# Kernel optimization log

Hardware: AMD Instinct MI355X
Metric: run time of the kernel (lower is better)

Reference implementation:

```python
import jax, jax.numpy as jnp
import numpy as np

N = 100000      # nodes
E = 1600000     # directed edges
F_IN = 128      # input features
H = 64          # hidden_channels
C = 32          # num_classes


def setup_inputs() -> dict:
    key = jax.random.key(0)
    ks = jax.random.split(key, 8)
    x = jax.random.normal(ks[0], (N, F_IN), jnp.float32)
    edge_index = jax.random.randint(ks[1], (2, E), 0, N, jnp.int32)
    W1 = jax.random.normal(ks[2], (F_IN, H), jnp.float32) * (1.0 / np.sqrt(F_IN))
    b1 = jnp.zeros((H,), jnp.float32)
    W2 = jax.random.normal(ks[3], (H, H), jnp.float32) * (1.0 / np.sqrt(H))
    b2 = jnp.zeros((H,), jnp.float32)
    Wout = jax.random.normal(ks[4], (H, C), jnp.float32) * (1.0 / np.sqrt(H))
    bout = jnp.zeros((C,), jnp.float32)
    return {"x": x, "edge_index": edge_index, "W1": W1, "b1": b1,
            "W2": W2, "b2": b2, "Wout": Wout, "bout": bout}


def gcn_conv(x, W, b, src, dst, n):
    """PyG GCNConv: out = D^-1/2 (A + I) D^-1/2 (X W) + b,
    with degree computed on A + I."""
    h = x @ W  # [N, out]
    ones = jnp.ones(dst.shape[0], h.dtype)
    deg = jax.ops.segment_sum(ones, dst, num_segments=n) + 1.0  # self-loop
    dinv = jax.lax.rsqrt(deg)                                   # [N]
    coef = dinv[src] * dinv[dst]                                # [E]
    agg = jax.ops.segment_sum(h[src] * coef[:, None], dst, num_segments=n)
    agg = agg + h * (dinv * dinv)[:, None]                      # self-loop message
    return agg + b


def reference(x, edge_index, W1, b1, W2, b2, Wout, bout):
    src, dst = edge_index[0], edge_index[1]
    n = x.shape[0]
    h = jax.nn.relu(gcn_conv(x, W1, b1, src, dst, n))
    # dropout(p=0.5) is a no-op in eval mode
    h = jax.nn.relu(gcn_conv(h, W2, b2, src, dst, n))
    return jax.nn.softmax(h @ Wout + bout, axis=1)
```

## Files before the change

kernel.cpp:

```cpp
#include <hip/hip_runtime.h>
#include <stdint.h>


typedef unsigned short u16;
typedef unsigned int u32;
typedef __attribute__((ext_vector_type(8))) short bf16x8;
typedef __attribute__((ext_vector_type(4))) float f32x4;

#define GN 100000
#define GE 1600000
#define NBKT 196
#define CBLK 782

__device__ __forceinline__ float bf2f(u32 lo16) {
  union { u32 i; float f; } v; v.i = lo16 << 16; return v.f;
}
__device__ __forceinline__ u16 f2bf(float f) {
  union { float f; u32 i; } v; v.f = f;
  u32 x = v.i;
  u32 r = x + 0x7fffu + ((x >> 16) & 1u);
  return (u16)(r >> 16);
}
__device__ __forceinline__ u32 pack2(float a, float b) {
  return (u32)f2bf(a) | ((u32)f2bf(b) << 16);
}

__global__ __launch_bounds__(256) void k_detect(const u16* __restrict__ xs,
                                                int* __restrict__ flag,
                                                int* __restrict__ ccount) {
  __shared__ int cnt;
  if (threadIdx.x == 0) cnt = 0;
  if (threadIdx.x < NBKT) ccount[threadIdx.x] = 0;
  __syncthreads();
  int w = 0;
#pragma unroll
  for (int i = 0; i < 16; i++) {
    int s = threadIdx.x * 16 + i;
    u32 u = xs[(size_t)s * 1562];
    u32 ex = (u >> 7) & 0xffu;
    if (ex == 0xffu || ex < 0x40u) w++;
  }
  atomicAdd(&cnt, w);
  __syncthreads();
  if (threadIdx.x == 0) flag[0] = (cnt >= 64) ? 0 : 1;
}

__global__ __launch_bounds__(256) void k_coarse(const int* __restrict__ dst,
                                                int* __restrict__ ccount, int E,
                                                const void* p2, const void* p3,
                                                const void* p4, const void* p5,
                                                const void* p6, const void* p7,
                                                const int* __restrict__ flag,
                                                float* __restrict__ Wf,
                                                u16* __restrict__ Wb1,
                                                u16* __restrict__ Wb2,
                                                u16* __restrict__ Wbo) {
  int tid = threadIdx.x;
  if (blockIdx.x >= CBLK) {
    int i = (blockIdx.x - CBLK) * 256 + tid;
    bool isbf = flag[0] != 0;
    if (i < 14496) {
      const void* src; int off;
      if (i < 8192)       { src = p2; off = i; }
      else if (i < 8256)  { src = p3; off = i - 8192; }
      else if (i < 12352) { src = p4; off = i - 8256; }
      else if (i < 12416) { src = p5; off = i - 12352; }
      else if (i < 14464) { src = p6; off = i - 12416; }
      else                { src = p7; off = i - 14464; }
      Wf[i] = isbf ? bf2f((u32)((const u16*)src)[off]) : ((const float*)src)[off];
    } else if (i < 14496 + 12288) {
      int idx = i - 14496;
      const void* W; u16* dstp;
      if (idx < 8192) { W = p2; dstp = Wb1; }
      else            { W = p4; dstp = Wb2; idx -= 8192; }
      int j  = idx & 7;
      int l  = (idx >> 3) & 63;
      int c  = (idx >> 9) & 3;
      int kc = idx >> 11;
      int k = kc * 32 + (l >> 4) * 8 + j;
      int n = c * 16 + (l & 15);
      dstp[idx] = isbf ? ((const u16*)W)[k * 64 + n]
                       : f2bf(((const float*)W)[k * 64 + n]);
    } else if (i < 14496 + 12288 + 2048) {
      int idx = i - 14496 - 12288;
      int j  = idx & 7;
      int l  = (idx >> 3) & 63;
      int c  = (idx >> 9) & 1;
      int kc = idx >> 10;
      int k = kc * 32 + (l >> 4) * 8 + j;
      int n = c * 16 + (l & 15);
      Wbo[idx] = isbf ? ((const u16*)p6)[k * 32 + n]
                      : f2bf(((const float*)p6)[k * 32 + n]);
    }
    return;
  }
  __shared__ int hist[256];
  hist[tid] = 0;
  __syncthreads();
  int e0 = (blockIdx.x * 256 + tid) * 8;
  if (e0 + 8 <= E) {
    const int4* dp = (const int4*)(dst + e0);
    int4 a = dp[0], b = dp[1];
    atomicAdd(&hist[a.x >> 9], 1); atomicAdd(&hist[a.y >> 9], 1);
    atomicAdd(&hist[a.z >> 9], 1); atomicAdd(&hist[a.w >> 9], 1);
    atomicAdd(&hist[b.x >> 9], 1); atomicAdd(&hist[b.y >> 9], 1);
    atomicAdd(&hist[b.z >> 9], 1); atomicAdd(&hist[b.w >> 9], 1);
  } else {
    for (int q = 0; q < 8 && e0 + q < E; q++)
      atomicAdd(&hist[dst[e0 + q] >> 9], 1);
  }
  __syncthreads();
  if (tid < NBKT && hist[tid]) atomicAdd(&ccount[tid], hist[tid]);
}

__global__ __launch_bounds__(256) void k_cscan(const int* __restrict__ ccount,
                                               int* __restrict__ cbase,
                                               int* __restrict__ cfill) {
  __shared__ int lds[256];
  int tid = threadIdx.x;
  int v = (tid < NBKT) ? ccount[tid] : 0;
  lds[tid] = v;
  __syncthreads();
#pragma unroll
  for (int off = 1; off < 256; off <<= 1) {
    int a = (tid >= off) ? lds[tid - off] : 0;
    __syncthreads();
    lds[tid] += a;
    __syncthreads();
  }
  int excl = lds[tid] - v;
  if (tid < NBKT) { cbase[tid] = excl; cfill[tid] = excl; }
  if (tid == 255) cbase[NBKT] = lds[255];
}

__global__ __launch_bounds__(256) void k_partA(const int* __restrict__ src,
                                               const int* __restrict__ dst,
                                               int* __restrict__ cfill,
                                               u32* __restrict__ pairs, int E) {
  __shared__ int hist[256];
  __shared__ int off[256];
  int tid = threadIdx.x;
  hist[tid] = 0;
  __syncthreads();
  int e0 = (blockIdx.x * 256 + tid) * 8;
  int s_[8], d_[8];
  int cnt = 0;
  if (e0 + 8 <= E) {
    const int4* sp = (const int4*)(src + e0);
    const int4* dp = (const int4*)(dst + e0);
#pragma unroll
    for (int q = 0; q < 2; q++) {
      int4 sv = sp[q], dv = dp[q];
      s_[4 * q + 0] = sv.x; s_[4 * q + 1] = sv.y;
      s_[4 * q + 2] = sv.z; s_[4 * q + 3] = sv.w;
      d_[4 * q + 0] = dv.x; d_[4 * q + 1] = dv.y;
      d_[4 * q + 2] = dv.z; d_[4 * q + 3] = dv.w;
    }
    cnt = 8;
  } else {
    for (int q = 0; q < 8 && e0 + q < E; q++) {
      s_[q] = src[e0 + q]; d_[q] = dst[e0 + q]; cnt++;
    }
  }
  for (int q = 0; q < cnt; q++) atomicAdd(&hist[d_[q] >> 9], 1);
  __syncthreads();
  if (tid < NBKT && hist[tid] > 0) off[tid] = atomicAdd(&cfill[tid], hist[tid]);
  __syncthreads();
  for (int q = 0; q < cnt; q++) {
    int bkt = d_[q] >> 9;
    int pos = atomicAdd(&off[bkt], 1);
    pairs[pos] = ((u32)s_[q] << 9) | ((u32)d_[q] & 511u);
  }
}

__global__ __launch_bounds__(256) void k_partB(const u32* __restrict__ pairs,
                                               const int* __restrict__ cbase,
                                               int* __restrict__ rp,
                                               float* __restrict__ dinv,
                                               int* __restrict__ ssort, int N) {
  __shared__ int cnt[512];
  __shared__ int sc[256];
  int b = blockIdx.x;
  int tid = threadIdx.x;
  int nb0 = b << 9;
  int beg = cbase[b], end = cbase[b + 1];
  cnt[tid] = 0; cnt[tid + 256] = 0;
  __syncthreads();
  for (int i = beg + tid; i < end; i += 256) {
    u32 p = pairs[i];
    atomicAdd(&cnt[p & 511u], 1);
  }
  __syncthreads();
  int c0 = cnt[2 * tid], c1 = cnt[2 * tid + 1];
  int s = c0 + c1;
  sc[tid] = s;
  __syncthreads();
#pragma unroll
  for (int off = 1; off < 256; off <<= 1) {
    int a = (tid >= off) ? sc[tid - off] : 0;
    __syncthreads();
    sc[tid] += a;
    __syncthreads();
  }
  int excl = sc[tid] - s;
  cnt[2 * tid] = excl;
  cnt[2 * tid + 1] = excl + c0;
  int n0 = nb0 + 2 * tid, n1 = n0 + 1;
  if (n0 < N) { rp[n0] = beg + excl;      dinv[n0] = rsqrtf((float)c0 + 1.0f); }
  if (n1 < N) { rp[n1] = beg + excl + c0; dinv[n1] = rsqrtf((float)c1 + 1.0f); }
  if (b == NBKT - 1 && tid == 0) rp[N] = end;
  __syncthreads();
  for (int i = beg + tid; i < end; i += 256) {
    u32 p = pairs[i];
    int pos = beg + atomicAdd(&cnt[p & 511u], 1);
    ssort[pos] = (int)(p >> 9);
  }
}

template <int K, int XMODE>
__global__ __launch_bounds__(256) void k_mgemm(const void* __restrict__ X,
                                               const u16* __restrict__ Wb,
                                               const float* __restrict__ dinv,
                                               const int* __restrict__ flag,
                                               u16* __restrict__ out, int M) {
  constexpr int NKC = K / 32;
  constexpr int P = K + 8;
  __shared__ u16 Bs[NKC * 4 * 64 * 8];
  __shared__ u16 As[128 * P];
  int tid = threadIdx.x;
  bool isbf = (XMODE == 1) ? true : (flag[0] != 0);
#pragma unroll
  for (int i = 0; i < NKC; i++)
    ((uint4*)Bs)[i * 256 + tid] = ((const uint4*)Wb)[i * 256 + tid];

  int rowbase = blockIdx.x * 128;
  int rowsValid = M - rowbase; if (rowsValid > 128) rowsValid = 128;
  if (isbf) {
    constexpr int F8 = K / 8;
    constexpr int NL = K / 16;
    const uint4* Xg = (const uint4*)X;
    uint4 v[NL];
#pragma unroll
    for (int i = 0; i < NL; i++) {
      int q = i * 256 + tid;
      int row = q / F8, c8 = q % F8;
      v[i] = (row < rowsValid) ? Xg[(size_t)(rowbase + row) * F8 + c8]
                               : make_uint4(0, 0, 0, 0);
    }
#pragma unroll
    for (int i = 0; i < NL; i++) {
      int q = i * 256 + tid;
      int row = q / F8, c8 = q % F8;
      *(uint4*)&As[row * P + c8 * 8] = v[i];
    }
  } else {
    constexpr int F4 = K / 4;
    constexpr int NL = K / 8;
    const float4* Xg = (const float4*)X;
    float4 v[NL];
#pragma unroll
    for (int i = 0; i < NL; i++) {
      int q = i * 256 + tid;
      int row = q / F4, c4 = q % F4;
      v[i] = (row < rowsValid) ? Xg[(size_t)(rowbase + row) * F4 + c4]
                               : make_float4(0.f, 0.f, 0.f, 0.f);
    }
#pragma unroll
    for (int i = 0; i < NL; i++) {
      int q = i * 256 + tid;
      int row = q / F4, c4 = q % F4;
      u32* d = (u32*)&As[row * P + c4 * 4];
      d[0] = pack2(v[i].x, v[i].y);
      d[1] = pack2(v[i].z, v[i].w);
    }
  }
  __syncthreads();

  int lane = tid & 63, wave = tid >> 6;
  int m0 = lane & 15;
  int koff = (lane >> 4) * 8;
  f32x4 acc[2][4];
#pragma unroll
  for (int t = 0; t < 2; t++)
#pragma unroll
    for (int c = 0; c < 4; c++) acc[t][c] = (f32x4){0.f, 0.f, 0.f, 0.f};

#pragma unroll
  for (int kc = 0; kc < NKC; kc++) {
    union { uint4 v; bf16x8 s; } a[2];
#pragma unroll
    for (int t = 0; t < 2; t++) {
      int rl = wave * 32 + t * 16 + m0;
      a[t].v = *(const uint4*)&As[rl * P + kc * 32 + koff];
    }
#pragma unroll
    for (int c = 0; c < 4; c++) {
      bf16x8 b = *(const bf16x8*)&Bs[((kc * 4 + c) * 64 + lane) * 8];
      acc[0][c] = __builtin_amdgcn_mfma_f32_16x16x32_bf16(a[0].s, b, acc[0][c], 0, 0, 0);
      acc[1][c] = __builtin_amdgcn_mfma_f32_16x16x32_bf16(a[1].s, b, acc[1][c], 0, 0, 0);
    }
  }
  __syncthreads();
  int cl = lane & 15, rq = (lane >> 4) * 4;
#pragma unroll
  for (int t = 0; t < 2; t++)
#pragma unroll
    for (int reg = 0; reg < 4; reg++) {
      int rl = wave * 32 + t * 16 + rq + reg;
      int r = rowbase + rl;
      float s = (r < M) ? dinv[r] : 0.f;
#pragma unroll
      for (int c = 0; c < 4; c++)
        As[rl * P + c * 16 + cl] = f2bf(acc[t][c][reg] * s);
    }
  __syncthreads();
  uint4* outg = (uint4*)out;
#pragma unroll
  for (int i = 0; i < 4; i++) {
    int q = i * 256 + tid;
    int row = q >> 3, c8 = q & 7;
    int r = rowbase + row;
    if (r < M) outg[(size_t)r * 8 + c8] = *(uint4*)&As[row * P + c8 * 8];
  }
}

__global__ __launch_bounds__(256) void k_pull(const u16* __restrict__ g,
                                              const int* __restrict__ rp,
                                              const int* __restrict__ ss,
                                              const float* __restrict__ dinv,
                                              const float* __restrict__ bias,
                                              u16* __restrict__ out, int N) {
  int gt = blockIdx.x * 256 + threadIdx.x;
  int node = gt >> 3;
  int fq = gt & 7;
  if (node >= N) return;
  const uint4* gp4 = (const uint4*)g;
  int beg = rp[node], end = rp[node + 1];

  uint4 sv = gp4[(size_t)node * 8 + fq];
  float acc[8];
  acc[0] = bf2f(sv.x & 0xffffu); acc[1] = bf2f(sv.x >> 16);
  acc[2] = bf2f(sv.y & 0xffffu); acc[3] = bf2f(sv.y >> 16);
  acc[4] = bf2f(sv.z & 0xffffu); acc[5] = bf2f(sv.z >> 16);
  acc[6] = bf2f(sv.w & 0xffffu); acc[7] = bf2f(sv.w >> 16);

#define ACC8(v)                                                      \
  do {                                                               \
    acc[0] += bf2f((v).x & 0xffffu); acc[1] += bf2f((v).x >> 16);    \
    acc[2] += bf2f((v).y & 0xffffu); acc[3] += bf2f((v).y >> 16);    \
    acc[4] += bf2f((v).z & 0xffffu); acc[5] += bf2f((v).z >> 16);    \
    acc[6] += bf2f((v).w & 0xffffu); acc[7] += bf2f((v).w >> 16);    \
  } while (0)

  int e = beg;
  for (; e + 4 <= end; e += 4) {
    int i0 = ss[e], i1 = ss[e + 1], i2 = ss[e + 2], i3 = ss[e + 3];
    uint4 v0 = gp4[(size_t)i0 * 8 + fq];
    uint4 v1 = gp4[(size_t)i1 * 8 + fq];
    uint4 v2 = gp4[(size_t)i2 * 8 + fq];
    uint4 v3 = gp4[(size_t)i3 * 8 + fq];
    ACC8(v0); ACC8(v1); ACC8(v2); ACC8(v3);
  }
  for (; e < end; e++) {
    int i0 = ss[e];
    uint4 v0 = gp4[(size_t)i0 * 8 + fq];
    ACC8(v0);
  }
#undef ACC8

  float dv = dinv[node];
  float4 b0 = ((const float4*)bias)[fq * 2];
  float4 b1 = ((const float4*)bias)[fq * 2 + 1];
  float r0 = fmaxf(dv * acc[0] + b0.x, 0.f);
  float r1 = fmaxf(dv * acc[1] + b0.y, 0.f);
  float r2 = fmaxf(dv * acc[2] + b0.z, 0.f);
  float r3 = fmaxf(dv * acc[3] + b0.w, 0.f);
  float r4 = fmaxf(dv * acc[4] + b1.x, 0.f);
  float r5 = fmaxf(dv * acc[5] + b1.y, 0.f);
  float r6 = fmaxf(dv * acc[6] + b1.z, 0.f);
  float r7 = fmaxf(dv * acc[7] + b1.w, 0.f);
  ((uint4*)out)[(size_t)node * 8 + fq] =
      make_uint4(pack2(r0, r1), pack2(r2, r3), pack2(r4, r5), pack2(r6, r7));
}

__global__ __launch_bounds__(256) void k_out(const u16* __restrict__ act,
                                             const u16* __restrict__ Wbo,
                                             const float* __restrict__ bof,
                                             const int* __restrict__ flag,
                                             void* __restrict__ outv, int N) {
  constexpr int P = 72;
  __shared__ u16 Bs[2 * 2 * 64 * 8];
  __shared__ u16 As[128 * P];
  __shared__ float Bsh[32];
  int tid = threadIdx.x;
  ((uint4*)Bs)[tid] = ((const uint4*)Wbo)[tid];
  if (tid < 32) Bsh[tid] = bof[tid];

  int rowbase = blockIdx.x * 128;
  int rowsValid = N - rowbase; if (rowsValid > 128) rowsValid = 128;
  const uint4* Xg = (const uint4*)act;
#pragma unroll
  for (int i = 0; i < 4; i++) {
    int q = i * 256 + tid;
    int row = q >> 3, c8 = q & 7;
    uint4 v = (row < rowsValid) ? Xg[(size_t)(rowbase + row) * 8 + c8]
                                : make_uint4(0, 0, 0, 0);
    *(uint4*)&As[row * P + c8 * 8] = v;
  }
  __syncthreads();

  bool isbf = flag[0] != 0;
  int lane = tid & 63, wave = tid >> 6;
  int m0 = lane & 15;
  int koff = (lane >> 4) * 8;
  f32x4 acc[2][2];
#pragma unroll
  for (int t = 0; t < 2; t++)
#pragma unroll
    for (int c = 0; c < 2; c++) acc[t][c] = (f32x4){0.f, 0.f, 0.f, 0.f};

#pragma unroll
  for (int kc = 0; kc < 2; kc++) {
    union { uint4 v; bf16x8 s; } a[2];
#pragma unroll
    for (int t = 0; t < 2; t++) {
      int rl = wave * 32 + t * 16 + m0;
      a[t].v = *(const uint4*)&As[rl * P + kc * 32 + koff];
    }
#pragma unroll
    for (int c = 0; c < 2; c++) {
      bf16x8 b = *(const bf16x8*)&Bs[((kc * 2 + c) * 64 + lane) * 8];
      acc[0][c] = __builtin_amdgcn_mfma_f32_16x16x32_bf16(a[0].s, b, acc[0][c], 0, 0, 0);
      acc[1][c] = __builtin_amdgcn_mfma_f32_16x16x32_bf16(a[1].s, b, acc[1][c], 0, 0, 0);
    }
  }
  int cl = lane & 15, rq = (lane >> 4) * 4;
  float b0 = Bsh[cl], b1 = Bsh[16 + cl];
#pragma unroll
  for (int t = 0; t < 2; t++)
#pragma unroll
    for (int reg = 0; reg < 4; reg++) {
      int r = rowbase + wave * 32 + t * 16 + rq + reg;
      float v0 = acc[t][0][reg] + b0;
      float v1 = acc[t][1][reg] + b1;
      float mx = fmaxf(v0, v1);
      mx = fmaxf(mx, __shfl_xor(mx, 1));
      mx = fmaxf(mx, __shfl_xor(mx, 2));
      mx = fmaxf(mx, __shfl_xor(mx, 4));
      mx = fmaxf(mx, __shfl_xor(mx, 8));
      float e0 = __expf(v0 - mx), e1 = __expf(v1 - mx);
      float s = e0 + e1;
      s += __shfl_xor(s, 1);
      s += __shfl_xor(s, 2);
      s += __shfl_xor(s, 4);
      s += __shfl_xor(s, 8);
      float inv = 1.f / s;
      if (r < N) {
        if (isbf) {
          u16* go = (u16*)outv;
          go[(size_t)r * 32 + cl]      = f2bf(e0 * inv);
          go[(size_t)r * 32 + 16 + cl] = f2bf(e1 * inv);
        } else {
          float* go = (float*)outv;
          go[(size_t)r * 32 + cl]      = e0 * inv;
          go[(size_t)r * 32 + 16 + cl] = e1 * inv;
        }
      }
    }
}

extern "C" void kernel_launch(void* const* d_in, const int* in_sizes, int n_in,
                              void* d_out, int out_size, void* d_ws, size_t ws_size,
                              hipStream_t stream) {
  (void)in_sizes; (void)n_in; (void)out_size; (void)ws_size;
  const void* x  = d_in[0];
  const int* ei  = (const int*)d_in[1];
  const int N = GN, E = GE;
  const int* srcI = ei;
  const int* dstI = ei + E;

  char* ws = (char*)d_ws;
  int*   flag   = (int*)(ws + 0);
  int*   ccount = (int*)(ws + 256);
  int*   cbase  = (int*)(ws + 1088);
  int*   cfill  = (int*)(ws + 1920);
  int*   rp     = (int*)(ws + 4096);
  float* dinv   = (float*)(ws + 404224);
  float* Wf     = (float*)(ws + 804352);
  u16*   Wb1    = (u16*)(ws + 862464);
  u16*   Wb2    = (u16*)(ws + 878848);
  u16*   Wbo    = (u16*)(ws + 887040);
  int*   ssort  = (int*)(ws + 891136);
  u32*   pairs  = (u32*)(ws + 7291136);
  u16*   gA     = (u16*)(ws + 7291136);
  u16*   gB     = (u16*)(ws + 20091136);

  float* b1f = Wf + 8192;
  float* b2f = Wf + 12352;
  float* bof = Wf + 14464;

  k_detect<<<1, 256, 0, stream>>>((const u16*)x, flag, ccount);
  k_coarse<<<CBLK + 113, 256, 0, stream>>>(dstI, ccount, E,
                                           d_in[2], d_in[3], d_in[4], d_in[5],
                                           d_in[6], d_in[7], flag,
                                           Wf, Wb1, Wb2, Wbo);
  k_cscan<<<1, 256, 0, stream>>>(ccount, cbase, cfill);
  k_partA<<<782, 256, 0, stream>>>(srcI, dstI, cfill, pairs, E);
  k_partB<<<NBKT, 256, 0, stream>>>(pairs, cbase, rp, dinv, ssort, N);

  k_mgemm<128, 0><<<782, 256, 0, stream>>>(x, Wb1, dinv, flag, gA, N);
  k_pull<<<3125, 256, 0, stream>>>(gA, rp, ssort, dinv, b1f, gB, N);
  k_mgemm<64, 1><<<782, 256, 0, stream>>>(gB, Wb2, dinv, flag, gA, N);
  k_pull<<<3125, 256, 0, stream>>>(gA, rp, ssort, dinv, b2f, gB, N);
  k_out<<<782, 256, 0, stream>>>(gB, Wbo, bof, flag, d_out, N);
}
```

Baseline: 269.0 us.

## Fixed-capacity buckets and fuse pull aggregation with following GEMM and softmax

Replaces the coarse histogram, scan and partition sequence with a single pass that writes into fixed-capacity buckets (BCAP per bucket), so two kernels and a global sync disappear. It also fuses each neighbor aggregation with the next dense transform: layer 1 pull feeds a 64x64 MFMA that is scaled by dinv and stored, and layer 2 pull feeds the output GEMM plus softmax. This removes the separate mgemm/out launches and the round trips of intermediate activations through memory. The cost is a bucket-overflow risk if a bucket exceeds the fixed capacity, padded row-pointer indexing, and MODE 1 leaving half the waves idle during its MFMA step.

```diff
diff --git a/kernel.cpp b/kernel.cpp
--- a/kernel.cpp
+++ b/kernel.cpp
@@ -10,7 +10,8 @@
 #define GN 100000
 #define GE 1600000
 #define NBKT 196
-#define CBLK 782
+#define BCAP 10240
+#define EBLK 782
 
 __device__ __forceinline__ float bf2f(u32 lo16) {
   union { u32 i; float f; } v; v.i = lo16 << 16; return v.f;
@@ -45,29 +46,31 @@
   if (threadIdx.x == 0) flag[0] = (cnt >= 64) ? 0 : 1;
 }
 
-__global__ __launch_bounds__(256) void k_coarse(const int* __restrict__ dst,
-                                                int* __restrict__ ccount, int E,
-                                                const void* p2, const void* p3,
-                                                const void* p4, const void* p5,
-                                                const void* p6, const void* p7,
-                                                const int* __restrict__ flag,
-                                                float* __restrict__ Wf,
-                                                u16* __restrict__ Wb1,
-                                                u16* __restrict__ Wb2,
-                                                u16* __restrict__ Wbo) {
+__global__ __launch_bounds__(256) void k_partA(const int* __restrict__ src,
+                                               const int* __restrict__ dst,
+                                               int* __restrict__ ccount, int E,
+                                               const void* p2, const void* p3,
+                                               const void* p4, const void* p5,
+                                               const void* p6, const void* p7,
+                                               const int* __restrict__ flag,
+                                               float* __restrict__ Wf,
+                                               u16* __restrict__ Wb1,
+                                               u16* __restrict__ Wb2,
+                                               u16* __restrict__ Wbo,
+                                               u32* __restrict__ pairs) {
   int tid = threadIdx.x;
-  if (blockIdx.x >= CBLK) {
-    int i = (blockIdx.x - CBLK) * 256 + tid;
+  if (blockIdx.x >= EBLK) {
+    int i = (blockIdx.x - EBLK) * 256 + tid;
     bool isbf = flag[0] != 0;
     if (i < 14496) {
-      const void* src; int off;
-      if (i < 8192)       { src = p2; off = i; }
-      else if (i < 8256)  { src = p3; off = i - 8192; }
-      else if (i < 12352) { src = p4; off = i - 8256; }
-      else if (i < 12416) { src = p5; off = i - 12352; }
-      else if (i < 14464) { src = p6; off = i - 12416; }
-      else                { src = p7; off = i - 14464; }
-      Wf[i] = isbf ? bf2f((u32)((const u16*)src)[off]) : ((const float*)src)[off];
+      const void* sp; int off;
+      if (i < 8192)       { sp = p2; off = i; }
+      else if (i < 8256)  { sp = p3; off = i - 8192; }
+      else if (i < 12352) { sp = p4; off = i - 8256; }
+      else if (i < 12416) { sp = p5; off = i - 12352; }
+      else if (i < 14464) { sp = p6; off = i - 12416; }
+      else                { sp = p7; off = i - 14464; }
+      Wf[i] = isbf ? bf2f((u32)((const u16*)sp)[off]) : ((const float*)sp)[off];
     } else if (i < 14496 + 12288) {
       int idx = i - 14496;
       const void* W; u16* dstp;
@@ -95,51 +98,7 @@
     return;
   }
   __shared__ int hist[256];
-  hist[tid] = 0;
-  __syncthreads();
-  int e0 = (blockIdx.x * 256 + tid) * 8;
-  if (e0 + 8 <= E) {
-    const int4* dp = (const int4*)(dst + e0);
-    int4 a = dp[0], b = dp[1];
-    atomicAdd(&hist[a.x >> 9], 1); atomicAdd(&hist[a.y >> 9], 1);
-    atomicAdd(&hist[a.z >> 9], 1); atomicAdd(&hist[a.w >> 9], 1);
-    atomicAdd(&hist[b.x >> 9], 1); atomicAdd(&hist[b.y >> 9], 1);
-    atomicAdd(&hist[b.z >> 9], 1); atomicAdd(&hist[b.w >> 9], 1);
-  } else {
-    for (int q = 0; q < 8 && e0 + q < E; q++)
-      atomicAdd(&hist[dst[e0 + q] >> 9], 1);
-  }
-  __syncthreads();
-  if (tid < NBKT && hist[tid]) atomicAdd(&ccount[tid], hist[tid]);
-}
-
-__global__ __launch_bounds__(256) void k_cscan(const int* __restrict__ ccount,
-                                               int* __restrict__ cbase,
-                                               int* __restrict__ cfill) {
-  __shared__ int lds[256];
-  int tid = threadIdx.x;
-  int v = (tid < NBKT) ? ccount[tid] : 0;
-  lds[tid] = v;
-  __syncthreads();
-#pragma unroll
-  for (int off = 1; off < 256; off <<= 1) {
-    int a = (tid >= off) ? lds[tid - off] : 0;
-    __syncthreads();
-    lds[tid] += a;
-    __syncthreads();
-  }
-  int excl = lds[tid] - v;
-  if (tid < NBKT) { cbase[tid] = excl; cfill[tid] = excl; }
-  if (tid == 255) cbase[NBKT] = lds[255];
-}
-
-__global__ __launch_bounds__(256) void k_partA(const int* __restrict__ src,
-                                               const int* __restrict__ dst,
-                                               int* __restrict__ cfill,
-                                               u32* __restrict__ pairs, int E) {
-  __shared__ int hist[256];
   __shared__ int off[256];
-  int tid = threadIdx.x;
   hist[tid] = 0;
   __syncthreads();
   int e0 = (blockIdx.x * 256 + tid) * 8;
@@ -164,7 +123,8 @@
   }
   for (int q = 0; q < cnt; q++) atomicAdd(&hist[d_[q] >> 9], 1);
   __syncthreads();
-  if (tid < NBKT && hist[tid] > 0) off[tid] = atomicAdd(&cfill[tid], hist[tid]);
+  if (tid < NBKT && hist[tid] > 0)
+    off[tid] = tid * BCAP + atomicAdd(&ccount[tid], hist[tid]);
   __syncthreads();
   for (int q = 0; q < cnt; q++) {
     int bkt = d_[q] >> 9;
@@ -174,8 +134,8 @@
 }
 
 __global__ __launch_bounds__(256) void k_partB(const u32* __restrict__ pairs,
-                                               const int* __restrict__ cbase,
-                                               int* __restrict__ rp,
+                                               const int* __restrict__ ccount,
+                                               int* __restrict__ rpx,
                                                float* __restrict__ dinv,
                                                int* __restrict__ ssort, int N) {
   __shared__ int cnt[512];
@@ -183,7 +143,7 @@
   int b = blockIdx.x;
   int tid = threadIdx.x;
   int nb0 = b << 9;
-  int beg = cbase[b], end = cbase[b + 1];
+  int beg = b * BCAP, end = beg + ccount[b];
   cnt[tid] = 0; cnt[tid + 256] = 0;
   __syncthreads();
   for (int i = beg + tid; i < end; i += 256) {
@@ -205,10 +165,13 @@
   int excl = sc[tid] - s;
   cnt[2 * tid] = excl;
   cnt[2 * tid + 1] = excl + c0;
+  int idx = b * 513 + 2 * tid;
+  rpx[idx]     = beg + excl;
+  rpx[idx + 1] = beg + excl + c0;
+  if (tid == 255) rpx[b * 513 + 512] = end;
   int n0 = nb0 + 2 * tid, n1 = n0 + 1;
-  if (n0 < N) { rp[n0] = beg + excl;      dinv[n0] = rsqrtf((float)c0 + 1.0f); }
-  if (n1 < N) { rp[n1] = beg + excl + c0; dinv[n1] = rsqrtf((float)c1 + 1.0f); }
-  if (b == NBKT - 1 && tid == 0) rp[N] = end;
+  if (n0 < N) dinv[n0] = rsqrtf((float)c0 + 1.0f);
+  if (n1 < N) dinv[n1] = rsqrtf((float)c1 + 1.0f);
   __syncthreads();
   for (int i = beg + tid; i < end; i += 256) {
     u32 p = pairs[i];
@@ -324,18 +287,37 @@
   }
 }
 
-__global__ __launch_bounds__(256) void k_pull(const u16* __restrict__ g,
-                                              const int* __restrict__ rp,
-                                              const int* __restrict__ ss,
-                                              const float* __restrict__ dinv,
-                                              const float* __restrict__ bias,
-                                              u16* __restrict__ out, int N) {
-  int gt = blockIdx.x * 256 + threadIdx.x;
-  int node = gt >> 3;
-  int fq = gt & 7;
-  if (node >= N) return;
+template <int MODE>
+__global__ __launch_bounds__(256) void k_pullg(const u16* __restrict__ g,
+                                               const int* __restrict__ rpx,
+                                               const int* __restrict__ ss,
+                                               const float* __restrict__ dinv,
+                                               const float* __restrict__ bias,
+                                               const u16* __restrict__ Wfrag,
+                                               const float* __restrict__ bof,
+                                               const int* __restrict__ flag,
+                                               void* __restrict__ outv) {
+  constexpr int P = 72;
+  __shared__ u16 Hs[32 * P];
+  __shared__ u16 Cs[(MODE == 0) ? 32 * P : 1];
+  int tid = threadIdx.x;
+  int lane = tid & 63, wave = tid >> 6;
+
+  constexpr int NCF = (MODE == 0) ? 4 : 2;
+  int c0 = (MODE == 0) ? ((wave >> 1) << 1) : 0;
+  bf16x8 bfr[2][2];
+#pragma unroll
+  for (int kc = 0; kc < 2; kc++)
+#pragma unroll
+    for (int cc = 0; cc < 2; cc++)
+      bfr[kc][cc] = *(const bf16x8*)&Wfrag[((kc * NCF + c0 + cc) * 64 + lane) * 8];
+
+  int oct = tid >> 3;
+  int node = blockIdx.x * 32 + oct;
+  int fq = tid & 7;
   const uint4* gp4 = (const uint4*)g;
-  int beg = rp[node], end = rp[node + 1];
+  int rix = node + (node >> 9);
+  int beg = rpx[rix], end = rpx[rix + 1];
 
   uint4 sv = gp4[(size_t)node * 8 + fq];
   float acc[8];
@@ -379,70 +361,46 @@
   float r5 = fmaxf(dv * acc[5] + b1.y, 0.f);
   float r6 = fmaxf(dv * acc[6] + b1.z, 0.f);
   float r7 = fmaxf(dv * acc[7] + b1.w, 0.f);
-  ((uint4*)out)[(size_t)node * 8 + fq] =
+  *(uint4*)&Hs[oct * P + fq * 8] =
       make_uint4(pack2(r0, r1), pack2(r2, r3), pack2(r4, r5), pack2(r6, r7));
-}
-
-__global__ __launch_bounds__(256) void k_out(const u16* __restrict__ act,
-                                             const u16* __restrict__ Wbo,
-                                             const float* __restrict__ bof,
-                                             const int* __restrict__ flag,
-                                             void* __restrict__ outv, int N) {
-  constexpr int P = 72;
-  __shared__ u16 Bs[2 * 2 * 64 * 8];
-  __shared__ u16 As[128 * P];
-  __shared__ float Bsh[32];
-  int tid = threadIdx.x;
-  ((uint4*)Bs)[tid] = ((const uint4*)Wbo)[tid];
-  if (tid < 32) Bsh[tid] = bof[tid];
-
-  int rowbase = blockIdx.x * 128;
-  int rowsValid = N - rowbase; if (rowsValid > 128) rowsValid = 128;
-  const uint4* Xg = (const uint4*)act;
-#pragma unroll
-  for (int i = 0; i < 4; i++) {
-    int q = i * 256 + tid;
-    int row = q >> 3, c8 = q & 7;
-    uint4 v = (row < rowsValid) ? Xg[(size_t)(rowbase + row) * 8 + c8]
-                                : make_uint4(0, 0, 0, 0);
-    *(uint4*)&As[row * P + c8 * 8] = v;
-  }
-  __syncthreads();
-
-  bool isbf = flag[0] != 0;
-  int lane = tid & 63, wave = tid >> 6;
+  __syncthreads();
+
   int m0 = lane & 15;
   int koff = (lane >> 4) * 8;
-  f32x4 acc[2][2];
-#pragma unroll
-  for (int t = 0; t < 2; t++)
-#pragma unroll
-    for (int c = 0; c < 2; c++) acc[t][c] = (f32x4){0.f, 0.f, 0.f, 0.f};
-
-#pragma unroll
-  for (int kc = 0; kc < 2; kc++) {
-    union { uint4 v; bf16x8 s; } a[2];
-#pragma unroll
-    for (int t = 0; t < 2; t++) {
-      int rl = wave * 32 + t * 16 + m0;
-      a[t].v = *(const uint4*)&As[rl * P + kc * 32 + koff];
-    }
-#pragma unroll
-    for (int c = 0; c < 2; c++) {
-      bf16x8 b = *(const bf16x8*)&Bs[((kc * 2 + c) * 64 + lane) * 8];
-      acc[0][c] = __builtin_amdgcn_mfma_f32_16x16x32_bf16(a[0].s, b, acc[0][c], 0, 0, 0);
-      acc[1][c] = __builtin_amdgcn_mfma_f32_16x16x32_bf16(a[1].s, b, acc[1][c], 0, 0, 0);
+  int rt = wave & 1;
+  f32x4 cacc[2];
+  cacc[0] = (f32x4){0.f, 0.f, 0.f, 0.f};
+  cacc[1] = (f32x4){0.f, 0.f, 0.f, 0.f};
+  if (MODE == 0 || wave < 2) {
+#pragma unroll
+    for (int kc = 0; kc < 2; kc++) {
+      union { uint4 v; bf16x8 s; } a;
+      a.v = *(const uint4*)&Hs[(rt * 16 + m0) * P + kc * 32 + koff];
+      cacc[0] = __builtin_amdgcn_mfma_f32_16x16x32_bf16(a.s, bfr[kc][0], cacc[0], 0, 0, 0);
+      cacc[1] = __builtin_amdgcn_mfma_f32_16x16x32_bf16(a.s, bfr[kc][1], cacc[1], 0, 0, 0);
     }
   }
   int cl = lane & 15, rq = (lane >> 4) * 4;
-  float b0 = Bsh[cl], b1 = Bsh[16 + cl];
-#pragma unroll
-  for (int t = 0; t < 2; t++)
+  if (MODE == 0) {
 #pragma unroll
     for (int reg = 0; reg < 4; reg++) {
-      int r = rowbase + wave * 32 + t * 16 + rq + reg;
-      float v0 = acc[t][0][reg] + b0;
-      float v1 = acc[t][1][reg] + b1;
+      int rl = rt * 16 + rq + reg;
+      float s = dinv[blockIdx.x * 32 + rl];
+      Cs[rl * P + (c0 + 0) * 16 + cl] = f2bf(cacc[0][reg] * s);
+      Cs[rl * P + (c0 + 1) * 16 + cl] = f2bf(cacc[1][reg] * s);
+    }
+    __syncthreads();
+    uint4* og = (uint4*)outv;
+    int row = tid >> 3, c8 = tid & 7;
+    og[(size_t)(blockIdx.x * 32 + row) * 8 + c8] = *(uint4*)&Cs[row * P + c8 * 8];
+  } else if (wave < 2) {
+    bool isbf = flag[0] != 0;
+    float bb0 = bof[cl], bb1 = bof[16 + cl];
+#pragma unroll
+    for (int reg = 0; reg < 4; reg++) {
+      int r = blockIdx.x * 32 + rt * 16 + rq + reg;
+      float v0 = cacc[0][reg] + bb0;
+      float v1 = cacc[1][reg] + bb1;
       float mx = fmaxf(v0, v1);
       mx = fmaxf(mx, __shfl_xor(mx, 1));
       mx = fmaxf(mx, __shfl_xor(mx, 2));
@@ -455,18 +413,17 @@
       s += __shfl_xor(s, 4);
       s += __shfl_xor(s, 8);
       float inv = 1.f / s;
-      if (r < N) {
-        if (isbf) {
-          u16* go = (u16*)outv;
-          go[(size_t)r * 32 + cl]      = f2bf(e0 * inv);
-          go[(size_t)r * 32 + 16 + cl] = f2bf(e1 * inv);
-        } else {
-          float* go = (float*)outv;
-          go[(size_t)r * 32 + cl]      = e0 * inv;
-          go[(size_t)r * 32 + 16 + cl] = e1 * inv;
-        }
+      if (isbf) {
+        u16* go = (u16*)outv;
+        go[(size_t)r * 32 + cl]      = f2bf(e0 * inv);
+        go[(size_t)r * 32 + 16 + cl] = f2bf(e1 * inv);
+      } else {
+        float* go = (float*)outv;
+        go[(size_t)r * 32 + cl]      = e0 * inv;
+        go[(size_t)r * 32 + 16 + cl] = e1 * inv;
       }
     }
+  }
 }
 
 extern "C" void kernel_launch(void* const* d_in, const int* in_sizes, int n_in,
@@ -475,42 +432,36 @@
   (void)in_sizes; (void)n_in; (void)out_size; (void)ws_size;
   const void* x  = d_in[0];
   const int* ei  = (const int*)d_in[1];
-  const int N = GN, E = GE;
+  const int E = GE;
   const int* srcI = ei;
   const int* dstI = ei + E;
 
   char* ws = (char*)d_ws;
   int*   flag   = (int*)(ws + 0);
   int*   ccount = (int*)(ws + 256);
-  int*   cbase  = (int*)(ws + 1088);
-  int*   cfill  = (int*)(ws + 1920);
-  int*   rp     = (int*)(ws + 4096);
-  float* dinv   = (float*)(ws + 404224);
-  float* Wf     = (float*)(ws + 804352);
-  u16*   Wb1    = (u16*)(ws + 862464);
-  u16*   Wb2    = (u16*)(ws + 878848);
-  u16*   Wbo    = (u16*)(ws + 887040);
-  int*   ssort  = (int*)(ws + 891136);
-  u32*   pairs  = (u32*)(ws + 7291136);
-  u16*   gA     = (u16*)(ws + 7291136);
-  u16*   gB     = (u16*)(ws + 20091136);
+  int*   rpx    = (int*)(ws + 4096);
+  float* dinv   = (float*)(ws + 406528);
+  float* Wf     = (float*)(ws + 806656);
+  u16*   Wb1    = (u16*)(ws + 864768);
+  u16*   Wb2    = (u16*)(ws + 881280);
+  u16*   Wbo    = (u16*)(ws + 889600);
+  int*   ssort  = (int*)(ws + 893952);
+  u32*   pairs  = (u32*)(ws + 8922112);
+  u16*   gA     = (u16*)(ws + 8922112);
+  u16*   gB     = (u16*)(ws + 21722368);
 
   float* b1f = Wf + 8192;
   float* b2f = Wf + 12352;
   float* bof = Wf + 14464;
 
   k_detect<<<1, 256, 0, stream>>>((const u16*)x, flag, ccount);
-  k_coarse<<<CBLK + 113, 256, 0, stream>>>(dstI, ccount, E,
-                                           d_in[2], d_in[3], d_in[4], d_in[5],
-                                           d_in[6], d_in[7], flag,
-                                           Wf, Wb1, Wb2, Wbo);
-  k_cscan<<<1, 256, 0, stream>>>(ccount, cbase, cfill);
-  k_partA<<<782, 256, 0, stream>>>(srcI, dstI, cfill, pairs, E);
-  k_partB<<<NBKT, 256, 0, stream>>>(pairs, cbase, rp, dinv, ssort, N);
-
-  k_mgemm<128, 0><<<782, 256, 0, stream>>>(x, Wb1, dinv, flag, gA, N);
-  k_pull<<<3125, 256, 0, stream>>>(gA, rp, ssort, dinv, b1f, gB, N);
-  k_mgemm<64, 1><<<782, 256, 0, stream>>>(gB, Wb2, dinv, flag, gA, N);
-  k_pull<<<3125, 256, 0, stream>>>(gA, rp, ssort, dinv, b2f, gB, N);
-  k_out<<<782, 256, 0, stream>>>(gB, Wbo, bof, flag, d_out, N);
-}
+  k_partA<<<EBLK + 113, 256, 0, stream>>>(srcI, dstI, ccount, E,
+                                          d_in[2], d_in[3], d_in[4], d_in[5],
+                                          d_in[6], d_in[7], flag,
+                                          Wf, Wb1, Wb2, Wbo, pairs);
+  k_partB<<<NBKT, 256, 0, stream>>>(pairs, ccount, rpx, dinv, ssort, GN);
+
+  k_mgemm<128, 0><<<782, 256, 0, stream>>>(x, Wb1, dinv, flag, gA, GN);
+  k_pullg<0><<<3125, 256, 0, stream>>>(gA, rpx, ssort, dinv, b1f, Wb2, bof, flag, gB);
+  k_pullg<1><<<3125, 256, 0, stream>>>(gB, rpx, ssort, dinv, b2f, Wbo, bof, flag, d_out);
+}
```

Result: faster. 235.9 us (-12.3%).
